# Kernel optimization log

Hardware: AMD Instinct MI355X
Metric: run time of the kernel (lower is better)

## Reference

```python
import jax, jax.numpy as jnp
import numpy as np

PRUNE_RATIO = 0.5
NOISE_SCALE = 0.1
MIXUP_ALPHA = 0.05
TEMPERATURE = 0.5
B, N, D = 32, 4096, 256


def setup_inputs() -> dict:
    key = jax.random.key(0)
    k1, k2, k3 = jax.random.split(key, 3)
    seq = jax.random.normal(k1, (B, N, D), dtype=jnp.float32)
    attn_weights = jax.random.uniform(k2, (B, N), dtype=jnp.float32)
    uniform_noise = jax.random.uniform(k3, (B, N), dtype=jnp.float32)
    return {"seq": seq, "attn_weights": attn_weights, "uniform_noise": uniform_noise}


def reference(seq, attn_weights, uniform_noise):
    b, n, d = seq.shape
    k = max(1, int(n * (1.0 - PRUNE_RATIO)))
    # training branch: gumbel noise from the provided uniform draw
    gumbel = -jnp.log(-jnp.log(uniform_noise + 1e-10) + 1e-10)
    noisy = attn_weights + NOISE_SCALE * gumbel                      # (B, N)
    soft = jax.nn.softmax(noisy / TEMPERATURE, axis=-1)              # (B, N)
    _, top_idx = jax.lax.top_k(soft, k)                              # (B, K) int32
    # gather selected tokens: (B, K, D)
    selected = jnp.take_along_axis(seq, top_idx[:, :, None], axis=1)
    # mixup: mean of the pruned (non-selected) tokens
    mask = jnp.ones((b, n), dtype=seq.dtype).at[
        jnp.arange(b)[:, None], top_idx
    ].set(0.0)                                                       # (B, N), 1 on pruned
    remaining_sum = jnp.einsum('bn,bnd->bd', mask, seq)              # (B, D)
    remaining_count = mask.sum(axis=1, keepdims=True) + 1e-10        # (B, 1)
    remaining_mean = remaining_sum / remaining_count                 # (B, D)
    return selected + MIXUP_ALPHA * remaining_mean[:, None, :]       # (B, K, D)
```

## Files before the change

### kernel.cpp

```cpp
#include <hip/hip_runtime.h>
#include <hip/hip_bf16.h>

#define B_ 32
#define N_ 4096
#define D_ 256
#define K_ 2048
#define SORT_THREADS 1024

__global__ __launch_bounds__(SORT_THREADS) void sort_kernel(
    const float* __restrict__ attn, const float* __restrict__ noise,
    int* __restrict__ sortedIdx, float* __restrict__ meanAccum) {
  __shared__ unsigned long long keys[N_];
  const int b = blockIdx.x;
  const int tid = threadIdx.x;

  for (int i = tid; i < N_; i += SORT_THREADS) {
    float u = noise[b * N_ + i];
    float a = attn[b * N_ + i];
    float x = __fadd_rn(u, 1e-10f);
    float l1 = (float)log((double)x);
    float inner = __fadd_rn(-l1, 1e-10f);
    float g = -(float)log((double)inner);
    float noisy = __fadd_rn(a, __fmul_rn(0.1f, g));
    unsigned int fb = __float_as_uint(noisy);
    fb = (fb & 0x80000000u) ? ~fb : (fb | 0x80000000u);
    keys[i] = ((unsigned long long)fb << 32) | (unsigned int)(~i);
  }
  __syncthreads();

  for (int k = 2; k <= N_; k <<= 1) {
    for (int j = k >> 1; j > 0; j >>= 1) {
      for (int t = tid; t < (N_ / 2); t += SORT_THREADS) {
        int i = ((t & ~(j - 1)) << 1) | (t & (j - 1));
        int ixj = i | j;
        unsigned long long a = keys[i];
        unsigned long long c = keys[ixj];
        bool descSeg = ((i & k) == 0);
        bool doSwap = descSeg ? (a < c) : (a > c);
        if (doSwap) { keys[i] = c; keys[ixj] = a; }
      }
      __syncthreads();
    }
  }

  for (int i = tid; i < N_; i += SORT_THREADS) {
    sortedIdx[b * N_ + i] = (int)(~(unsigned int)(keys[i] & 0xFFFFFFFFu));
  }
  for (int d = tid; d < D_; d += SORT_THREADS) meanAccum[b * D_ + d] = 0.0f;
}

__global__ __launch_bounds__(256) void mean_kernel(
    const float* __restrict__ seq, const int* __restrict__ sortedIdx,
    float* __restrict__ meanAccum) {
  const int b = blockIdx.y;
  const int chunk = blockIdx.x;
  const int tid = threadIdx.x;
  const int dv = tid & 63;
  const int sub = tid >> 6;
  const int base = b * N_ + K_ + chunk * 128;

  float4 acc = make_float4(0.f, 0.f, 0.f, 0.f);
  for (int r = sub; r < 128; r += 4) {
    int idx = sortedIdx[base + r];
    const float4* row = (const float4*)(seq + ((size_t)b * N_ + idx) * D_);
    float4 v = row[dv];
    acc.x += v.x; acc.y += v.y; acc.z += v.z; acc.w += v.w;
  }

  __shared__ float4 red[4][64];
  red[sub][dv] = acc;
  __syncthreads();
  if (sub == 0) {
    float4 s0 = red[0][dv], s1 = red[1][dv], s2 = red[2][dv], s3 = red[3][dv];
    float sx = s0.x + s1.x + s2.x + s3.x;
    float sy = s0.y + s1.y + s2.y + s3.y;
    float sz = s0.z + s1.z + s2.z + s3.z;
    float sw = s0.w + s1.w + s2.w + s3.w;
    float* dst = meanAccum + b * D_ + dv * 4;
    atomicAdd(dst + 0, sx);
    atomicAdd(dst + 1, sy);
    atomicAdd(dst + 2, sz);
    atomicAdd(dst + 3, sw);
  }
}

__global__ __launch_bounds__(256) void out_kernel(
    const float* __restrict__ seq, const int* __restrict__ sortedIdx,
    const float* __restrict__ meanAccum, float* __restrict__ out) {
  const unsigned int t = blockIdx.x * 256u + threadIdx.x;
  const int dv = t & 63;
  const int j = (t >> 6) & (K_ - 1);
  const int b = t >> 17;

  int idx = sortedIdx[b * N_ + j];
  float4 v = ((const float4*)(seq + ((size_t)b * N_ + idx) * D_))[dv];
  float4 m = ((const float4*)(meanAccum + b * D_))[dv];
  const float inv_cnt = 1.0f / 2048.0f;
  float4 o;
  o.x = v.x + 0.05f * (m.x * inv_cnt);
  o.y = v.y + 0.05f * (m.y * inv_cnt);
  o.z = v.z + 0.05f * (m.z * inv_cnt);
  o.w = v.w + 0.05f * (m.w * inv_cnt);
  ((float4*)out)[t] = o;
}

extern "C" void kernel_launch(void* const* d_in, const int* in_sizes, int n_in,
                              void* d_out, int out_size, void* d_ws, size_t ws_size,
                              hipStream_t stream) {
  const float* seq  = (const float*)d_in[0];
  const float* attn = (const float*)d_in[1];
  const float* nois = (const float*)d_in[2];
  float* out = (float*)d_out;

  int* sortedIdx   = (int*)d_ws;
  float* meanAccum = (float*)((char*)d_ws + (size_t)B_ * N_ * 4);

  sort_kernel<<<B_, SORT_THREADS, 0, stream>>>(attn, nois, sortedIdx, meanAccum);
  mean_kernel<<<dim3(16, B_), 256, 0, stream>>>(seq, sortedIdx, meanAccum);
  const int total4 = B_ * K_ * (D_ / 4);
  out_kernel<<<total4 / 256, 256, 0, stream>>>(seq, sortedIdx, meanAccum, out);
}
```

Before: 280.3 us.

## Replace per-batch bitonic sort with parallel rank-by-counting across many blocks

Splits key generation into its own fully parallel kernel and replaces the single-block-per-batch bitonic sort with a rank kernel in which each thread counts how many keys exceed its own and scatters its index to that rank. The aim is to remove the many barrier-separated sort stages and the use of only one block per batch, which leaves most compute units idle. The trade is quadratic comparison work per batch plus an extra kernel launch and a global round-trip for the keys.

```diff
diff --git a/kernel.cpp b/kernel.cpp
--- a/kernel.cpp
+++ b/kernel.cpp
@@ -5,48 +5,45 @@
 #define N_ 4096
 #define D_ 256
 #define K_ 2048
-#define SORT_THREADS 1024
 
-__global__ __launch_bounds__(SORT_THREADS) void sort_kernel(
+__global__ __launch_bounds__(256) void key_kernel(
     const float* __restrict__ attn, const float* __restrict__ noise,
-    int* __restrict__ sortedIdx, float* __restrict__ meanAccum) {
-  __shared__ unsigned long long keys[N_];
-  const int b = blockIdx.x;
-  const int tid = threadIdx.x;
+    unsigned long long* __restrict__ keys, float* __restrict__ meanAccum) {
+  const int t = blockIdx.x * 256 + threadIdx.x;
+  float u = noise[t];
+  float a = attn[t];
+  float x = __fadd_rn(u, 1e-10f);
+  float l1 = (float)log((double)x);
+  float inner = __fadd_rn(-l1, 1e-10f);
+  float g = -(float)log((double)inner);
+  float noisy = __fadd_rn(a, __fmul_rn(0.1f, g));
+  unsigned int fb = __float_as_uint(noisy);
+  fb = (fb & 0x80000000u) ? ~fb : (fb | 0x80000000u);
+  int i = t & (N_ - 1);
+  keys[t] = ((unsigned long long)fb << 32) | (unsigned int)(~i);
+  if (t < B_ * D_) meanAccum[t] = 0.0f;
+}
 
-  for (int i = tid; i < N_; i += SORT_THREADS) {
-    float u = noise[b * N_ + i];
-    float a = attn[b * N_ + i];
-    float x = __fadd_rn(u, 1e-10f);
-    float l1 = (float)log((double)x);
-    float inner = __fadd_rn(-l1, 1e-10f);
-    float g = -(float)log((double)inner);
-    float noisy = __fadd_rn(a, __fmul_rn(0.1f, g));
-    unsigned int fb = __float_as_uint(noisy);
-    fb = (fb & 0x80000000u) ? ~fb : (fb | 0x80000000u);
-    keys[i] = ((unsigned long long)fb << 32) | (unsigned int)(~i);
-  }
+__global__ __launch_bounds__(256) void rank_kernel(
+    const unsigned long long* __restrict__ keys, int* __restrict__ sortedIdx) {
+  __shared__ __align__(16) unsigned long long lk[N_];
+  const int b = blockIdx.y;
+
+  const ulonglong2* gk = (const ulonglong2*)(keys + (size_t)b * N_);
+  ulonglong2* lk2 = (ulonglong2*)lk;
+  for (int i = threadIdx.x; i < N_ / 2; i += 256) lk2[i] = gk[i];
   __syncthreads();
 
-  for (int k = 2; k <= N_; k <<= 1) {
-    for (int j = k >> 1; j > 0; j >>= 1) {
-      for (int t = tid; t < (N_ / 2); t += SORT_THREADS) {
-        int i = ((t & ~(j - 1)) << 1) | (t & (j - 1));
-        int ixj = i | j;
-        unsigned long long a = keys[i];
-        unsigned long long c = keys[ixj];
-        bool descSeg = ((i & k) == 0);
-        bool doSwap = descSeg ? (a < c) : (a > c);
-        if (doSwap) { keys[i] = c; keys[ixj] = a; }
-      }
-      __syncthreads();
-    }
+  const int i = blockIdx.x * 256 + threadIdx.x;
+  const unsigned long long ki = lk[i];
+  int rank = 0;
+#pragma unroll 8
+  for (int j = 0; j < N_ / 2; ++j) {
+    ulonglong2 v = lk2[j];
+    rank += (v.x > ki);
+    rank += (v.y > ki);
   }
-
-  for (int i = tid; i < N_; i += SORT_THREADS) {
-    sortedIdx[b * N_ + i] = (int)(~(unsigned int)(keys[i] & 0xFFFFFFFFu));
-  }
-  for (int d = tid; d < D_; d += SORT_THREADS) meanAccum[b * D_ + d] = 0.0f;
+  sortedIdx[(size_t)b * N_ + rank] = i;
 }
 
 __global__ __launch_bounds__(256) void mean_kernel(
@@ -114,8 +111,11 @@
 
   int* sortedIdx   = (int*)d_ws;
   float* meanAccum = (float*)((char*)d_ws + (size_t)B_ * N_ * 4);
+  unsigned long long* keys =
+      (unsigned long long*)((char*)d_ws + (size_t)B_ * N_ * 4 + (size_t)B_ * D_ * 4);
 
-  sort_kernel<<<B_, SORT_THREADS, 0, stream>>>(attn, nois, sortedIdx, meanAccum);
+  key_kernel<<<(B_ * N_) / 256, 256, 0, stream>>>(attn, nois, keys, meanAccum);
+  rank_kernel<<<dim3(N_ / 256, B_), 256, 0, stream>>>(keys, sortedIdx);
   mean_kernel<<<dim3(16, B_), 256, 0, stream>>>(seq, sortedIdx, meanAccum);
   const int total4 = B_ * K_ * (D_ / 4);
   out_kernel<<<total4 / 256, 256, 0, stream>>>(seq, sortedIdx, meanAccum, out);
```

Result: slower. 293.6 us (+4.7%).
